# Kernel optimization log

Measured on AMD Instinct MI355X. Metric: run time of the kernel, lower is better.

## Reference

```python
import jax, jax.numpy as jnp
import numpy as np
import math

NUM_HEADS = 16


def setup_inputs() -> dict:
    key = jax.random.key(0)
    ks = jax.random.split(key, 6)
    L, B, E = 1024, 4, 1024
    D = E // NUM_HEADS
    return {
        "query": jax.random.normal(ks[0], (L, B, E), dtype=jnp.float32),
        "relpos_mat": jax.random.normal(ks[1], (L, D), dtype=jnp.float32),
        "in_proj_weight": jax.random.normal(ks[2], (3 * E, E), dtype=jnp.float32) * 0.02,
        "in_proj_bias": jax.random.normal(ks[3], (3 * E,), dtype=jnp.float32) * 0.02,
        "out_proj_weight": jax.random.normal(ks[4], (E, E), dtype=jnp.float32) * 0.02,
        "out_proj_bias": jax.random.normal(ks[5], (E,), dtype=jnp.float32) * 0.02,
    }


def _skew(qe):
    # qe: (B*H, L, L). Music-Transformer skew trick.
    sz = qe.shape[1]
    mask = jnp.flip(jnp.triu(jnp.ones((sz, sz), dtype=qe.dtype)), axis=0)
    qe = qe * mask
    qe = jnp.pad(qe, ((0, 0), (0, 0), (1, 0)))  # (BH, L, L+1)
    qe = qe.reshape(qe.shape[0], sz + 1, sz)     # (BH, L+1, L)
    return qe[:, 1:, :]                          # (BH, L, L)


def reference(query, relpos_mat, in_proj_weight, in_proj_bias, out_proj_weight, out_proj_bias):
    L, B, E = query.shape
    H = NUM_HEADS
    D = E // H

    # packed QKV projection (self-attention path)
    qkv = query @ in_proj_weight.T + in_proj_bias  # (L, B, 3E)
    q, k, v = jnp.split(qkv, 3, axis=-1)

    def to_bh(x):  # (L, B, E) -> (B*H, L, D)
        return x.reshape(L, B * H, D).transpose(1, 0, 2)

    q = to_bh(q) / math.sqrt(D)
    k = to_bh(k)
    v = to_bh(v)

    attn = jnp.einsum('bld,bmd->blm', q, k)  # (BH, L, L)

    # valid relative embeddings: last L rows
    start = max(0, relpos_mat.shape[0] - L)
    er = relpos_mat[start:, :]               # (L, D)
    qe = jnp.einsum('hld,md->hlm', q, er)    # (BH, L, L)
    srel = _skew(qe)

    attn = jax.nn.softmax(attn + srel, axis=-1)
    out = jnp.einsum('blm,bmd->bld', attn, v)            # (BH, L, D)
    out = out.transpose(1, 0, 2).reshape(L, B, E)         # (L, B, E)
    out = out @ out_proj_weight.T + out_proj_bias
    return out
```

## Files before the change

kernel.cpp:

```cpp
#include <hip/hip_runtime.h>
#include <hip/hip_bf16.h>

#define SL 1024
#define BB 4
#define EE 1024
#define HH 16
#define DD 64
#define BHC 64
#define M1 4096

typedef __bf16 bf16x8 __attribute__((ext_vector_type(8)));
typedef __bf16 bf16x4 __attribute__((ext_vector_type(4)));
typedef float f32x4 __attribute__((ext_vector_type(4)));

typedef __attribute__((address_space(3))) unsigned int lds_u32;
typedef const __attribute__((address_space(1))) unsigned int g_u32;

__device__ __forceinline__ f32x4 mfma16(bf16x8 a, bf16x8 b, f32x4 c) {
    return __builtin_amdgcn_mfma_f32_16x16x32_bf16(a, b, c, 0, 0, 0);
}

#define FR(buf, row, chunk) (*(const bf16x8*)&(buf)[(row) * 64 + (((chunk) ^ ((row) & 7))) * 8])

__global__ __launch_bounds__(256) void prep_k(const float* __restrict__ query,
                                              const float* __restrict__ w_in,
                                              const float* __restrict__ w_out,
                                              const float* __restrict__ rel,
                                              __bf16* __restrict__ qA,
                                              __bf16* __restrict__ winb,
                                              __bf16* __restrict__ woutb,
                                              __bf16* __restrict__ erfp) {
    int bid = blockIdx.x, tid = threadIdx.x;
    const float* src;
    __bf16* dst;
    int idx;
    if (bid < 4096)      { src = query; dst = qA;    idx = (bid * 256 + tid) * 4; }
    else if (bid < 7168) { src = w_in;  dst = winb;  idx = ((bid - 4096) * 256 + tid) * 4; }
    else if (bid < 8192) { src = w_out; dst = woutb; idx = ((bid - 7168) * 256 + tid) * 4; }
    else {
        int e4 = ((bid - 8192) * 256 + tid) * 4;
        int r = e4 >> 6, d = e4 & 63;
        float4 v = *(const float4*)&rel[(1023 - r) * 64 + d];
        bf16x4 o;
        o[0] = (__bf16)v.x; o[1] = (__bf16)v.y; o[2] = (__bf16)v.z; o[3] = (__bf16)v.w;
        *(bf16x4*)&erfp[e4] = o;
        return;
    }
    float4 v = *(const float4*)&src[idx];
    bf16x4 o;
    o[0] = (__bf16)v.x; o[1] = (__bf16)v.y; o[2] = (__bf16)v.z; o[3] = (__bf16)v.w;
    *(bf16x4*)&dst[idx] = o;
}

#define BMt 128
#define BNt 128
#define BKt 32
__global__ __launch_bounds__(256) void gemm_bt(const __bf16* __restrict__ A,
                                               const __bf16* __restrict__ Bm,
                                               const float* __restrict__ bias,
                                               int M, int N, int K, int mode,
                                               __bf16* __restrict__ q_ws,
                                               __bf16* __restrict__ k_ws,
                                               __bf16* __restrict__ vT_ws,
                                               float* __restrict__ outf) {
    __shared__ __bf16 As[BMt * BKt];
    __shared__ __bf16 Bs[BNt * BKt];
    int tid = threadIdx.x;
    int wave = tid >> 6, lane = tid & 63;
    int quad = lane >> 4, c = lane & 15;
    int ntiles = N / BNt;
    int bx = blockIdx.x % ntiles, by = blockIdx.x / ntiles;
    int m0 = by * BMt, n0 = bx * BNt;
    int wm = (wave >> 1) * 64, wn = (wave & 1) * 64;
    int srow = lane >> 2, scol = (lane & 3) * 8;

    f32x4 acc[4][4] = {};
    for (int k0 = 0; k0 < K; k0 += BKt) {
        __syncthreads();
#pragma unroll
        for (int n = 0; n < 2; ++n) {
            int r0 = 32 * wave + 16 * n;
            const __bf16* ga = &A[(long)(m0 + r0 + srow) * K + k0 + scol];
            const __bf16* gb = &Bm[(long)(n0 + r0 + srow) * K + k0 + scol];
            __builtin_amdgcn_global_load_lds((g_u32*)ga, (lds_u32*)&As[r0 * BKt], 16, 0, 0);
            __builtin_amdgcn_global_load_lds((g_u32*)gb, (lds_u32*)&Bs[r0 * BKt], 16, 0, 0);
        }
        __syncthreads();
        bf16x8 af[4], bfr[4];
#pragma unroll
        for (int t = 0; t < 4; ++t) {
            af[t]  = *(const bf16x8*)&As[(wm + t * 16 + c) * BKt + quad * 8];
            bfr[t] = *(const bf16x8*)&Bs[(wn + t * 16 + c) * BKt + quad * 8];
        }
#pragma unroll
        for (int mt = 0; mt < 4; ++mt)
#pragma unroll
            for (int nt = 0; nt < 4; ++nt)
                acc[mt][nt] = mfma16(af[mt], bfr[nt], acc[mt][nt]);
    }

    if (mode == 1) {
#pragma unroll
        for (int mt = 0; mt < 4; ++mt)
#pragma unroll
            for (int nt = 0; nt < 4; ++nt) {
                int nn = n0 + wn + nt * 16 + c;
                float bv = bias[nn];
#pragma unroll
                for (int i = 0; i < 4; ++i) {
                    int mm = m0 + wm + mt * 16 + quad * 4 + i;
                    outf[(long)mm * N + nn] = acc[mt][nt][i] + bv;
                }
            }
        return;
    }
    __syncthreads();
    __bf16* slab = ((wave < 2) ? As : Bs) + (wave & 1) * 2048;
    int nnb = n0 + wn;
    int which = nnb >> 10;
    int hh = (nnb & 1023) >> 6;
    float scale = (which == 0) ? 0.125f : 1.0f;
#pragma unroll
    for (int mt = 0; mt < 4; ++mt) {
#pragma unroll
        for (int nt = 0; nt < 4; ++nt) {
            float bv = bias[nnb + nt * 16 + c];
#pragma unroll
            for (int i = 0; i < 4; ++i)
                slab[(quad * 4 + i) * 72 + nt * 16 + c] =
                    (__bf16)((acc[mt][nt][i] + bv) * scale);
        }
        if (which < 2) {
            int mm = m0 + wm + mt * 16 + c;
            int l = mm >> 2, bb = mm & 3;
            __bf16* dstp = ((which == 0) ? q_ws : k_ws) +
                           ((long)(bb * 16 + hh) * 1024 + l) * 64;
            bf16x8 t0 = *(const bf16x8*)&slab[c * 72 + quad * 8];
            bf16x8 t1 = *(const bf16x8*)&slab[c * 72 + 32 + quad * 8];
            *(bf16x8*)&dstp[quad * 8] = t0;
            *(bf16x8*)&dstp[32 + quad * 8] = t1;
        } else {
            int d = quad * 16 + c;
            __bf16 tmp[16];
#pragma unroll
            for (int jr = 0; jr < 16; ++jr) tmp[jr] = slab[jr * 72 + d];
            int L0 = (m0 + wm + mt * 16) >> 2;
#pragma unroll
            for (int bs = 0; bs < 4; ++bs) {
                bf16x4 pk;
                pk[0] = tmp[bs]; pk[1] = tmp[4 + bs];
                pk[2] = tmp[8 + bs]; pk[3] = tmp[12 + bs];
                *(bf16x4*)&vT_ws[((long)(bs * 16 + hh) * 64 + d) * 1024 + L0] = pk;
            }
        }
    }
}

#define RSTn 72
#define RSLOT (32 * RSTn)
__global__ __launch_bounds__(256, 2) void attn_kernel(const __bf16* __restrict__ q_ws,
                                                      const __bf16* __restrict__ k_ws,
                                                      const __bf16* __restrict__ vT_ws,
                                                      const __bf16* __restrict__ erf,
                                                      __bf16* __restrict__ O_flat) {
    __shared__ __bf16 Ks[2][4096];
    __shared__ __bf16 Vs[2][4096];
    __shared__ __bf16 Ring[4][2][RSLOT];

    int tid = threadIdx.x;
    int w = tid >> 6, lane = tid & 63;
    int q = lane >> 4, c = lane & 15;
    int bid = blockIdx.x;
    int x = bid & 7, ii = bid >> 3;
    int bh = x * 8 + (ii >> 3);
    int blk_l0 = (ii & 7) * 128;
    int b = bh >> 4, h = bh & 15;
    int l0w = blk_l0 + w * 32;

    __bf16* RW = &Ring[w][0][0];

    const __bf16* qp = q_ws + ((long)bh * 1024 + l0w) * 64;
    bf16x8 qf0[2], qf1[2];
    qf0[0] = *(const bf16x8*)&qp[c * 64 + q * 8];
    qf1[0] = *(const bf16x8*)&qp[c * 64 + 32 + q * 8];
    qf0[1] = *(const bf16x8*)&qp[(16 + c) * 64 + q * 8];
    qf1[1] = *(const bf16x8*)&qp[(16 + c) * 64 + 32 + q * 8];

    const __bf16* kbase = k_ws + (long)bh * 65536;
    const __bf16* vbase = vT_ws + (long)bh * 65536;

    int sr[2], sc[2], ldo[2];
#pragma unroll
    for (int n = 0; n < 2; ++n) {
        int sidx = w * 128 + n * 64 + lane;
        sr[n] = sidx >> 3;
        sc[n] = (sidx & 7) ^ (sr[n] & 7);
        ldo[n] = (w * 128 + n * 64) * 8;
    }

#pragma unroll
    for (int n = 0; n < 2; ++n) {
        __builtin_amdgcn_global_load_lds((g_u32*)(kbase + 15 * 4096 + sr[n] * 64 + sc[n] * 8),
                                         (lds_u32*)&Ks[1][ldo[n]], 16, 0, 0);
        __builtin_amdgcn_global_load_lds((g_u32*)(vbase + sr[n] * 1024 + 15 * 64 + sc[n] * 8),
                                         (lds_u32*)&Vs[1][ldo[n]], 16, 0, 0);
    }
    __syncthreads();

    f32x4 O[2][4] = {};
    float l_run[2] = {0.f, 0.f};

    for (int kt = 15; kt >= 0; --kt) {
        int p = kt & 1;
        if (kt > 0) {
#pragma unroll
            for (int n = 0; n < 2; ++n) {
                __builtin_amdgcn_global_load_lds(
                    (g_u32*)(kbase + (kt - 1) * 4096 + sr[n] * 64 + sc[n] * 8),
                    (lds_u32*)&Ks[p ^ 1][ldo[n]], 16, 0, 0);
                __builtin_amdgcn_global_load_lds(
                    (g_u32*)(vbase + sr[n] * 1024 + (kt - 1) * 64 + sc[n] * 8),
                    (lds_u32*)&Vs[p ^ 1][ldo[n]], 16, 0, 0);
            }
        }
        int rmax = l0w + 31 - kt * 64;
        int t1 = rmax >> 6;
        bf16x8 ea0[4], ea1[4];
        if (rmax >= 0) {
            const __bf16* ep = erf + (long)t1 * 4096;
#pragma unroll
            for (int s = 0; s < 4; ++s) {
                ea0[s] = *(const bf16x8*)&ep[(16 * s + c) * 64 + q * 8];
                ea1[s] = *(const bf16x8*)&ep[(16 * s + c) * 64 + 32 + q * 8];
            }
        }
        const __bf16* Kp = Ks[p];
        bf16x8 ka0[4], ka1[4];
#pragma unroll
        for (int s = 0; s < 4; ++s) {
            int row = 16 * s + c;
            ka0[s] = FR(Kp, row, q);
            ka1[s] = FR(Kp, row, 4 + q);
        }
        f32x4 S[2][4];
#pragma unroll
        for (int g = 0; g < 2; ++g)
#pragma unroll
            for (int s = 0; s < 4; ++s) {
                f32x4 acc = {0.f, 0.f, 0.f, 0.f};
                acc = mfma16(ka0[s], qf0[g], acc);
                acc = mfma16(ka1[s], qf1[g], acc);
                S[g][s] = acc;
            }
        if (rmax >= 0) {
            __bf16* rt = RW + (t1 & 1) * RSLOT;
#pragma unroll
            for (int g = 0; g < 2; ++g)
#pragma unroll
                for (int s = 0; s < 4; ++s) {
                    f32x4 ar = {0.f, 0.f, 0.f, 0.f};
                    ar = mfma16(ea0[s], qf0[g], ar);
                    ar = mfma16(ea1[s], qf1[g], ar);
                    bf16x4 pk;
#pragma unroll
                    for (int i = 0; i < 4; ++i) pk[i] = (__bf16)ar[i];
                    *(bf16x4*)&rt[(g * 16 + c) * RSTn + 16 * s + 4 * q] = pk;
                }
#pragma unroll
            for (int g = 0; g < 2; ++g) {
                int rb = l0w + g * 16 + c - kt * 64 - 4 * q;
#pragma unroll
                for (int s = 0; s < 4; ++s)
#pragma unroll
                    for (int i = 0; i < 4; ++i) {
                        int r = rb - 16 * s - i;
                        if (r >= 0)
                            S[g][s][i] += (float)RW[((r >> 6) & 1) * RSLOT +
                                                    (g * 16 + c) * RSTn + (r & 63)];
                    }
            }
        }
        int pslot = (rmax >= 0) ? ((t1 & 1) ^ 1) : 1;
#pragma unroll
        for (int g = 0; g < 2; ++g) {
            float ps[4];
#pragma unroll
            for (int s = 0; s < 4; ++s) {
                float a = __expf(S[g][s][0]), b2 = __expf(S[g][s][1]);
                float c2 = __expf(S[g][s][2]), d2 = __expf(S[g][s][3]);
                S[g][s][0] = a; S[g][s][1] = b2; S[g][s][2] = c2; S[g][s][3] = d2;
                ps[s] = (a + b2) + (c2 + d2);
            }
            l_run[g] += (ps[0] + ps[1]) + (ps[2] + ps[3]);
        }
        __bf16* PW = RW + pslot * RSLOT;
#pragma unroll
        for (int g = 0; g < 2; ++g)
#pragma unroll
            for (int s = 0; s < 4; ++s) {
                bf16x4 pk;
#pragma unroll
                for (int i = 0; i < 4; ++i) pk[i] = (__bf16)S[g][s][i];
                *(bf16x4*)&PW[(g * 16 + c) * RSTn + 16 * s + 4 * q] = pk;
            }
        const __bf16* Vp = Vs[p];
        bf16x8 va0[4], va1[4];
#pragma unroll
        for (int s = 0; s < 4; ++s) {
            int row = 16 * s + c;
            va0[s] = FR(Vp, row, q);
            va1[s] = FR(Vp, row, 4 + q);
        }
        bf16x8 pa0[2], pa1[2];
#pragma unroll
        for (int g = 0; g < 2; ++g) {
            pa0[g] = *(const bf16x8*)&PW[(g * 16 + c) * RSTn + q * 8];
            pa1[g] = *(const bf16x8*)&PW[(g * 16 + c) * RSTn + 32 + q * 8];
        }
#pragma unroll
        for (int g = 0; g < 2; ++g)
#pragma unroll
            for (int s = 0; s < 4; ++s) {
                O[g][s] = mfma16(va0[s], pa0[g], O[g][s]);
                O[g][s] = mfma16(va1[s], pa1[g], O[g][s]);
            }
        __syncthreads();
    }
#pragma unroll
    for (int g = 0; g < 2; ++g) {
        float tot = l_run[g];
        tot += __shfl_xor(tot, 16);
        tot += __shfl_xor(tot, 32);
        float rs = 1.0f / tot;
        long row = (long)(l0w + g * 16 + c) * 4 + b;
#pragma unroll
        for (int s = 0; s < 4; ++s) {
            bf16x4 ov;
#pragma unroll
            for (int i = 0; i < 4; ++i) ov[i] = (__bf16)(O[g][s][i] * rs);
            *(bf16x4*)&O_flat[row * 1024 + h * 64 + 16 * s + 4 * q] = ov;
        }
    }
}

extern "C" void kernel_launch(void* const* d_in, const int* in_sizes, int n_in,
                              void* d_out, int out_size, void* d_ws, size_t ws_size,
                              hipStream_t stream) {
    const float* query  = (const float*)d_in[0];
    const float* relpos = (const float*)d_in[1];
    const float* w_in   = (const float*)d_in[2];
    const float* b_in   = (const float*)d_in[3];
    const float* w_out  = (const float*)d_in[4];
    const float* b_out  = (const float*)d_in[5];
    float* out = (float*)d_out;

    char* ws = (char*)d_ws;
    size_t off = 0;
    auto alloc = [&](size_t bytes) {
        void* p = ws + off;
        off += (bytes + 255) & ~(size_t)255;
        return p;
    };
    __bf16* qA    = (__bf16*)alloc((size_t)M1 * EE * 2);
    __bf16* winb  = (__bf16*)alloc((size_t)3 * EE * EE * 2);
    __bf16* woutb = (__bf16*)alloc((size_t)EE * EE * 2);
    __bf16* erfp  = (__bf16*)alloc((size_t)SL * DD * 2);
    __bf16* q_ws  = (__bf16*)alloc((size_t)BHC * SL * DD * 2);
    __bf16* k_ws  = (__bf16*)alloc((size_t)BHC * SL * DD * 2);
    __bf16* vT_ws = (__bf16*)alloc((size_t)BHC * SL * DD * 2);
    __bf16* O_flat= (__bf16*)alloc((size_t)M1 * EE * 2);

    prep_k<<<8256, 256, 0, stream>>>(query, w_in, w_out, relpos,
                                     qA, winb, woutb, erfp);

    gemm_bt<<<(3072 / BNt) * (M1 / BMt), 256, 0, stream>>>(
        qA, winb, b_in, M1, 3072, EE, 0, q_ws, k_ws, vT_ws, nullptr);

    attn_kernel<<<512, 256, 0, stream>>>(q_ws, k_ws, vT_ws, erfp, O_flat);

    gemm_bt<<<(1024 / BNt) * (M1 / BMt), 256, 0, stream>>>(
        O_flat, woutb, b_out, M1, 1024, EE, 1, nullptr, nullptr, nullptr, out);
}
```

Measured before the change: 221.3 us.

## Stage relpos tiles in LDS, single-buffer V, split output GEMM with narrower tiles

The attention kernel now loads the relative-position embedding tile for the whole block into a double-buffered LDS array, shared by all four waves, instead of each wave reading it from global memory. V becomes single-buffered and is loaded in the same iteration it is used, with an added mid-loop barrier. The output projection moves to a dedicated kernel with 128x64 tiles, giving 512 blocks instead of 256 to fill more CUs. The trade is less V prefetch overlap and an extra barrier per iteration.

```diff
diff --git a/kernel.cpp b/kernel.cpp
--- a/kernel.cpp
+++ b/kernel.cpp
@@ -55,14 +55,13 @@
 #define BMt 128
 #define BNt 128
 #define BKt 32
-__global__ __launch_bounds__(256) void gemm_bt(const __bf16* __restrict__ A,
-                                               const __bf16* __restrict__ Bm,
-                                               const float* __restrict__ bias,
-                                               int M, int N, int K, int mode,
-                                               __bf16* __restrict__ q_ws,
-                                               __bf16* __restrict__ k_ws,
-                                               __bf16* __restrict__ vT_ws,
-                                               float* __restrict__ outf) {
+__global__ __launch_bounds__(256) void gemm_qkv(const __bf16* __restrict__ A,
+                                                const __bf16* __restrict__ Bm,
+                                                const float* __restrict__ bias,
+                                                __bf16* __restrict__ q_ws,
+                                                __bf16* __restrict__ k_ws,
+                                                __bf16* __restrict__ vT_ws) {
+    const int M = M1, N = 3072, K = EE;
     __shared__ __bf16 As[BMt * BKt];
     __shared__ __bf16 Bs[BNt * BKt];
     int tid = threadIdx.x;
@@ -97,22 +96,6 @@
 #pragma unroll
             for (int nt = 0; nt < 4; ++nt)
                 acc[mt][nt] = mfma16(af[mt], bfr[nt], acc[mt][nt]);
-    }
-
-    if (mode == 1) {
-#pragma unroll
-        for (int mt = 0; mt < 4; ++mt)
-#pragma unroll
-            for (int nt = 0; nt < 4; ++nt) {
-                int nn = n0 + wn + nt * 16 + c;
-                float bv = bias[nn];
-#pragma unroll
-                for (int i = 0; i < 4; ++i) {
-                    int mm = m0 + wm + mt * 16 + quad * 4 + i;
-                    outf[(long)mm * N + nn] = acc[mt][nt][i] + bv;
-                }
-            }
-        return;
     }
     __syncthreads();
     __bf16* slab = ((wave < 2) ? As : Bs) + (wave & 1) * 2048;
@@ -156,6 +139,63 @@
     }
 }
 
+__global__ __launch_bounds__(256) void gemm_out(const __bf16* __restrict__ A,
+                                                const __bf16* __restrict__ Bm,
+                                                const float* __restrict__ bias,
+                                                float* __restrict__ outf) {
+    const int N = 1024, K = EE;
+    __shared__ __bf16 As[BMt * BKt];
+    __shared__ __bf16 Bs[64 * BKt];
+    int tid = threadIdx.x;
+    int wave = tid >> 6, lane = tid & 63;
+    int quad = lane >> 4, c = lane & 15;
+    int bx = blockIdx.x & 15, by = blockIdx.x >> 4;
+    int m0 = by * BMt, n0 = bx * 64;
+    int wm = (wave >> 1) * 64, wn = (wave & 1) * 32;
+    int srow = lane >> 2, scol = (lane & 3) * 8;
+
+    f32x4 acc[4][2] = {};
+    for (int k0 = 0; k0 < K; k0 += BKt) {
+        __syncthreads();
+#pragma unroll
+        for (int n = 0; n < 2; ++n) {
+            int r0 = 32 * wave + 16 * n;
+            const __bf16* ga = &A[(long)(m0 + r0 + srow) * K + k0 + scol];
+            __builtin_amdgcn_global_load_lds((g_u32*)ga, (lds_u32*)&As[r0 * BKt], 16, 0, 0);
+        }
+        {
+            int r0 = 16 * wave;
+            const __bf16* gb = &Bm[(long)(n0 + r0 + srow) * K + k0 + scol];
+            __builtin_amdgcn_global_load_lds((g_u32*)gb, (lds_u32*)&Bs[r0 * BKt], 16, 0, 0);
+        }
+        __syncthreads();
+        bf16x8 af[4], bfr[2];
+#pragma unroll
+        for (int t = 0; t < 4; ++t)
+            af[t] = *(const bf16x8*)&As[(wm + t * 16 + c) * BKt + quad * 8];
+#pragma unroll
+        for (int t = 0; t < 2; ++t)
+            bfr[t] = *(const bf16x8*)&Bs[(wn + t * 16 + c) * BKt + quad * 8];
+#pragma unroll
+        for (int mt = 0; mt < 4; ++mt)
+#pragma unroll
+            for (int nt = 0; nt < 2; ++nt)
+                acc[mt][nt] = mfma16(af[mt], bfr[nt], acc[mt][nt]);
+    }
+#pragma unroll
+    for (int mt = 0; mt < 4; ++mt)
+#pragma unroll
+        for (int nt = 0; nt < 2; ++nt) {
+            int nn = n0 + wn + nt * 16 + c;
+            float bv = bias[nn];
+#pragma unroll
+            for (int i = 0; i < 4; ++i) {
+                int mm = m0 + wm + mt * 16 + quad * 4 + i;
+                outf[(long)mm * N + nn] = acc[mt][nt][i] + bv;
+            }
+        }
+}
+
 #define RSTn 72
 #define RSLOT (32 * RSTn)
 __global__ __launch_bounds__(256, 2) void attn_kernel(const __bf16* __restrict__ q_ws,
@@ -164,7 +204,8 @@
                                                       const __bf16* __restrict__ erf,
                                                       __bf16* __restrict__ O_flat) {
     __shared__ __bf16 Ks[2][4096];
-    __shared__ __bf16 Vs[2][4096];
+    __shared__ __bf16 Vs[4096];
+    __shared__ __bf16 Es[2][4096];
     __shared__ __bf16 Ring[4][2][RSLOT];
 
     int tid = threadIdx.x;
@@ -199,12 +240,9 @@
     }
 
 #pragma unroll
-    for (int n = 0; n < 2; ++n) {
+    for (int n = 0; n < 2; ++n)
         __builtin_amdgcn_global_load_lds((g_u32*)(kbase + 15 * 4096 + sr[n] * 64 + sc[n] * 8),
                                          (lds_u32*)&Ks[1][ldo[n]], 16, 0, 0);
-        __builtin_amdgcn_global_load_lds((g_u32*)(vbase + sr[n] * 1024 + 15 * 64 + sc[n] * 8),
-                                         (lds_u32*)&Vs[1][ldo[n]], 16, 0, 0);
-    }
     __syncthreads();
 
     f32x4 O[2][4] = {};
@@ -214,25 +252,24 @@
         int p = kt & 1;
         if (kt > 0) {
 #pragma unroll
-            for (int n = 0; n < 2; ++n) {
+            for (int n = 0; n < 2; ++n)
                 __builtin_amdgcn_global_load_lds(
                     (g_u32*)(kbase + (kt - 1) * 4096 + sr[n] * 64 + sc[n] * 8),
                     (lds_u32*)&Ks[p ^ 1][ldo[n]], 16, 0, 0);
+        }
+#pragma unroll
+        for (int n = 0; n < 2; ++n)
+            __builtin_amdgcn_global_load_lds(
+                (g_u32*)(vbase + sr[n] * 1024 + kt * 64 + sc[n] * 8),
+                (lds_u32*)&Vs[ldo[n]], 16, 0, 0);
+        int rmaxB = blk_l0 + 127 - kt * 64;
+        if (rmaxB >= 0) {
+            int tB = rmaxB >> 6;
+#pragma unroll
+            for (int n = 0; n < 2; ++n)
                 __builtin_amdgcn_global_load_lds(
-                    (g_u32*)(vbase + sr[n] * 1024 + (kt - 1) * 64 + sc[n] * 8),
-                    (lds_u32*)&Vs[p ^ 1][ldo[n]], 16, 0, 0);
-            }
-        }
-        int rmax = l0w + 31 - kt * 64;
-        int t1 = rmax >> 6;
-        bf16x8 ea0[4], ea1[4];
-        if (rmax >= 0) {
-            const __bf16* ep = erf + (long)t1 * 4096;
-#pragma unroll
-            for (int s = 0; s < 4; ++s) {
-                ea0[s] = *(const bf16x8*)&ep[(16 * s + c) * 64 + q * 8];
-                ea1[s] = *(const bf16x8*)&ep[(16 * s + c) * 64 + 32 + q * 8];
-            }
+                    (g_u32*)(erf + tB * 4096 + sr[n] * 64 + sc[n] * 8),
+                    (lds_u32*)&Es[tB & 1][ldo[n]], 16, 0, 0);
         }
         const __bf16* Kp = Ks[p];
         bf16x8 ka0[4], ka1[4];
@@ -252,7 +289,18 @@
                 acc = mfma16(ka1[s], qf1[g], acc);
                 S[g][s] = acc;
             }
+        __syncthreads();
+        int rmax = l0w + 31 - kt * 64;
+        int t1 = rmax >> 6;
         if (rmax >= 0) {
+            const __bf16* Ep = Es[t1 & 1];
+            bf16x8 ea0[4], ea1[4];
+#pragma unroll
+            for (int s = 0; s < 4; ++s) {
+                int row = 16 * s + c;
+                ea0[s] = FR(Ep, row, q);
+                ea1[s] = FR(Ep, row, 4 + q);
+            }
             __bf16* rt = RW + (t1 & 1) * RSLOT;
 #pragma unroll
             for (int g = 0; g < 2; ++g)
@@ -303,13 +351,12 @@
                 for (int i = 0; i < 4; ++i) pk[i] = (__bf16)S[g][s][i];
                 *(bf16x4*)&PW[(g * 16 + c) * RSTn + 16 * s + 4 * q] = pk;
             }
-        const __bf16* Vp = Vs[p];
         bf16x8 va0[4], va1[4];
 #pragma unroll
         for (int s = 0; s < 4; ++s) {
             int row = 16 * s + c;
-            va0[s] = FR(Vp, row, q);
-            va1[s] = FR(Vp, row, 4 + q);
+            va0[s] = FR(Vs, row, q);
+            va1[s] = FR(Vs, row, 4 + q);
         }
         bf16x8 pa0[2], pa1[2];
 #pragma unroll
@@ -373,11 +420,10 @@
     prep_k<<<8256, 256, 0, stream>>>(query, w_in, w_out, relpos,
                                      qA, winb, woutb, erfp);
 
-    gemm_bt<<<(3072 / BNt) * (M1 / BMt), 256, 0, stream>>>(
-        qA, winb, b_in, M1, 3072, EE, 0, q_ws, k_ws, vT_ws, nullptr);
+    gemm_qkv<<<(3072 / BNt) * (M1 / BMt), 256, 0, stream>>>(
+        qA, winb, b_in, q_ws, k_ws, vT_ws);
 
     attn_kernel<<<512, 256, 0, stream>>>(q_ws, k_ws, vT_ws, erfp, O_flat);
 
-    gemm_bt<<<(1024 / BNt) * (M1 / BMt), 256, 0, stream>>>(
-        O_flat, woutb, b_out, M1, 1024, EE, 1, nullptr, nullptr, nullptr, out);
-}
+    gemm_out<<<512, 256, 0, stream>>>(O_flat, woutb, b_out, out);
+}
```

Measured after the change: 205.0 us. -7.4%, faster.
